# Optimization experiments

Hardware: AMD Instinct MI355X
Metric: run time of the kernel (lower is better)

Reference implementation:

```python
import jax, jax.numpy as jnp
import numpy as np
from jax import lax

DN = ('NCHW', 'OIHW', 'NCHW')


def setup_inputs() -> dict:
    key = jax.random.key(0)
    ks = jax.random.split(key, 5)
    B, C, H, W = 32, 512, 56, 56
    R = 16
    return {
        'x': jax.random.normal(ks[0], (B, C, H, W), jnp.float32),
        'w1': jax.random.normal(ks[1], (1, 3, 3, 3), jnp.float32) * 0.2,   # shared conv over (y1,y2,y4) triplet
        'w2': jax.random.normal(ks[2], (1, 1, 3, 3), jnp.float32) * 0.2,   # shared depthwise conv
        'fc1_w': jax.random.normal(ks[3], (C // R, C), jnp.float32) * 0.05,
        'fc2_w': jax.random.normal(ks[4], (C, C // R), jnp.float32) * 0.05,
    }


def reference(x, w1, w2, fc1_w, fc2_w):
    b, c, h, w = x.shape
    # multi-scale adaptive average pooling (H,W divisible by 4) + nearest upsample to 4x4
    y1 = jnp.broadcast_to(x.mean(axis=(2, 3), keepdims=True), (b, c, 4, 4))      # pool1 -> interp x4
    y2 = x.reshape(b, c, 2, h // 2, 2, w // 2).mean(axis=(3, 5))                 # [b,c,2,2]
    y2 = jnp.repeat(jnp.repeat(y2, 2, axis=2), 2, axis=3)                        # nearest interp x2 -> 4x4
    y4 = x.reshape(b, c, 4, h // 4, 4, w // 4).mean(axis=(3, 5))                 # [b,c,4,4]
    # ShareGroupConv(3c->c): out channel j sees channels (j, c+j, 2c+j) = (y1_j, y2_j, y4_j)
    t = jnp.stack([y1, y2, y4], axis=2).reshape(b * c, 3, 4, 4)
    z = lax.conv_general_dilated(t, w1, (1, 1), 'VALID', dimension_numbers=DN)   # [b*c,1,2,2]
    # ShareGroupConv(c->c, k=3, pad=1, stride=3): shared per-channel conv, 2x2 -> 1x1
    z = lax.conv_general_dilated(z, w2, (3, 3), [(1, 1), (1, 1)], dimension_numbers=DN)
    s = z.reshape(b, c)
    s = jax.nn.relu(s @ fc1_w.T) @ fc2_w.T
    s = jax.nn.sigmoid(s).reshape(b, c, 1, 1)
    return x * s
```

## Files before the change

### kernel.cpp

```cpp
#include <hip/hip_runtime.h>
#include <math.h>

#define Bn 32
#define Cn 512
#define Hn 56
#define Wn 56
#define HW (Hn*Wn)
#define NPLANE (Bn*Cn)

__global__ __launch_bounds__(256) void pool_conv_kernel(
    const float* __restrict__ x,
    const float* __restrict__ w1,
    const float* __restrict__ w2,
    float* __restrict__ s0)
{
    __shared__ float plane[HW];
    __shared__ float rs[Hn * 4];
    __shared__ float y4[16];

    const int bc = blockIdx.x;
    const int t  = threadIdx.x;
    const float* src = x + (size_t)bc * HW;

    for (int f = t; f < HW / 4; f += 256)
        ((float4*)plane)[f] = ((const float4*)src)[f];
    __syncthreads();

    if (t < Hn * 4) {
        const int h = t >> 2, j = t & 3;
        const float* row = plane + h * Wn + j * 14;
        float s = 0.f;
        #pragma unroll
        for (int e = 0; e < 14; ++e) s += row[e];
        rs[h * 4 + j] = s;
    }
    __syncthreads();

    if (t < 16) {
        const int i = t >> 2, j = t & 3;
        float s = 0.f;
        #pragma unroll
        for (int r = 0; r < 14; ++r) s += rs[(i * 14 + r) * 4 + j];
        y4[i * 4 + j] = s * (1.0f / 196.0f);
    }
    __syncthreads();

    if (t == 0) {
        float y2[2][2];
        #pragma unroll
        for (int p = 0; p < 2; ++p)
            #pragma unroll
            for (int q = 0; q < 2; ++q)
                y2[p][q] = 0.25f * (y4[(2*p)*4 + 2*q]   + y4[(2*p)*4 + 2*q+1]
                                  + y4[(2*p+1)*4 + 2*q] + y4[(2*p+1)*4 + 2*q+1]);
        const float y1 = 0.25f * (y2[0][0] + y2[0][1] + y2[1][0] + y2[1][1]);

        float z[2][2];
        #pragma unroll
        for (int oy = 0; oy < 2; ++oy)
            #pragma unroll
            for (int ox = 0; ox < 2; ++ox) {
                float acc = 0.f;
                #pragma unroll
                for (int ky = 0; ky < 3; ++ky)
                    #pragma unroll
                    for (int kx = 0; kx < 3; ++kx) {
                        const int yy = oy + ky, xx = ox + kx;
                        acc += y1                  * w1[0*9 + ky*3 + kx];
                        acc += y2[yy >> 1][xx >> 1] * w1[1*9 + ky*3 + kx];
                        acc += y4[yy*4 + xx]        * w1[2*9 + ky*3 + kx];
                    }
                z[oy][ox] = acc;
            }

        const float out = z[0][0] * w2[1*3+1] + z[0][1] * w2[1*3+2]
                        + z[1][0] * w2[2*3+1] + z[1][1] * w2[2*3+2];
        s0[bc] = out;
    }
}

__global__ __launch_bounds__(256) void fc_kernel(
    const float* __restrict__ s0,
    const float* __restrict__ fc1,
    const float* __restrict__ fc2,
    float* __restrict__ s)
{
    __shared__ float sv[Cn];
    __shared__ float hv[32];
    const int b = blockIdx.x;
    const int t = threadIdx.x;

    for (int c = t; c < Cn; c += 256) sv[c] = s0[b * Cn + c];
    __syncthreads();

    {
        const int r = t >> 3, lane8 = t & 7;
        float acc = 0.f;
        for (int c = lane8; c < Cn; c += 8) acc += sv[c] * fc1[r * Cn + c];
        acc += __shfl_xor(acc, 1);
        acc += __shfl_xor(acc, 2);
        acc += __shfl_xor(acc, 4);
        if (lane8 == 0) hv[r] = fmaxf(acc, 0.f);
    }
    __syncthreads();

    for (int c = t; c < Cn; c += 256) {
        float acc = 0.f;
        #pragma unroll
        for (int r = 0; r < 32; ++r) acc += hv[r] * fc2[c * 32 + r];
        s[b * Cn + c] = 1.0f / (1.0f + expf(-acc));
    }
}

__global__ __launch_bounds__(256) void scale_kernel(
    const float* __restrict__ x,
    const float* __restrict__ s,
    float* __restrict__ out)
{
    const int n4 = NPLANE * HW / 4;
    const int stride = gridDim.x * blockDim.x;
    for (int i = blockIdx.x * blockDim.x + threadIdx.x; i < n4; i += stride) {
        float4 v = ((const float4*)x)[i];
        const float sc = s[i / (HW / 4)];
        v.x *= sc; v.y *= sc; v.z *= sc; v.w *= sc;
        ((float4*)out)[i] = v;
    }
}

extern "C" void kernel_launch(void* const* d_in, const int* in_sizes, int n_in,
                              void* d_out, int out_size, void* d_ws, size_t ws_size,
                              hipStream_t stream) {
    const float* x   = (const float*)d_in[0];
    const float* w1  = (const float*)d_in[1];
    const float* w2  = (const float*)d_in[2];
    const float* fc1 = (const float*)d_in[3];
    const float* fc2 = (const float*)d_in[4];
    float* out = (float*)d_out;

    float* s0 = (float*)d_ws;
    float* s  = s0 + NPLANE;

    pool_conv_kernel<<<NPLANE, 256, 0, stream>>>(x, w1, w2, s0);
    fc_kernel<<<Bn, 256, 0, stream>>>(s0, fc1, fc2, s);
    scale_kernel<<<2048, 256, 0, stream>>>(x, s, out);
}
```

Baseline: 126.4 us.

## Fuse FC excitation into the scale kernel with per-block channel groups

Merges the squeeze FC layers and the broadcast scale into one kernel. Each of 2048 blocks recomputes the FC1 hidden vector for its batch, computes sigmoid scales for its 8 channels, then scales those 8 planes using nontemporal stores. This removes one launch, the intermediate scale buffer and the per-element index division. In exchange, FC1 is computed redundantly 64 times per batch.

```diff
diff --git a/kernel.cpp b/kernel.cpp
--- a/kernel.cpp
+++ b/kernel.cpp
@@ -7,6 +7,9 @@
 #define Wn 56
 #define HW (Hn*Wn)
 #define NPLANE (Bn*Cn)
+#define F4_PER_PLANE (HW/4)
+
+typedef float f4 __attribute__((ext_vector_type(4)));
 
 __global__ __launch_bounds__(256) void pool_conv_kernel(
     const float* __restrict__ x,
@@ -22,8 +25,8 @@
     const int t  = threadIdx.x;
     const float* src = x + (size_t)bc * HW;
 
-    for (int f = t; f < HW / 4; f += 256)
-        ((float4*)plane)[f] = ((const float4*)src)[f];
+    for (int f = t; f < F4_PER_PLANE; f += 256)
+        ((f4*)plane)[f] = ((const f4*)src)[f];
     __syncthreads();
 
     if (t < Hn * 4) {
@@ -66,29 +69,32 @@
                     #pragma unroll
                     for (int kx = 0; kx < 3; ++kx) {
                         const int yy = oy + ky, xx = ox + kx;
-                        acc += y1                  * w1[0*9 + ky*3 + kx];
+                        acc += y1                   * w1[0*9 + ky*3 + kx];
                         acc += y2[yy >> 1][xx >> 1] * w1[1*9 + ky*3 + kx];
                         acc += y4[yy*4 + xx]        * w1[2*9 + ky*3 + kx];
                     }
                 z[oy][ox] = acc;
             }
 
-        const float out = z[0][0] * w2[1*3+1] + z[0][1] * w2[1*3+2]
-                        + z[1][0] * w2[2*3+1] + z[1][1] * w2[2*3+2];
-        s0[bc] = out;
+        s0[bc] = z[0][0] * w2[1*3+1] + z[0][1] * w2[1*3+2]
+               + z[1][0] * w2[2*3+1] + z[1][1] * w2[2*3+2];
     }
 }
 
-__global__ __launch_bounds__(256) void fc_kernel(
+__global__ __launch_bounds__(256) void fc_scale_kernel(
+    const float* __restrict__ x,
     const float* __restrict__ s0,
     const float* __restrict__ fc1,
     const float* __restrict__ fc2,
-    float* __restrict__ s)
+    float* __restrict__ out)
 {
     __shared__ float sv[Cn];
     __shared__ float hv[32];
-    const int b = blockIdx.x;
-    const int t = threadIdx.x;
+    __shared__ float scl[8];
+
+    const int b  = blockIdx.x >> 6;
+    const int kk = blockIdx.x & 63;
+    const int t  = threadIdx.x;
 
     for (int c = t; c < Cn; c += 256) sv[c] = s0[b * Cn + c];
     __syncthreads();
@@ -104,26 +110,26 @@
     }
     __syncthreads();
 
-    for (int c = t; c < Cn; c += 256) {
+    if (t < 8) {
+        const int c = kk * 8 + t;
         float acc = 0.f;
         #pragma unroll
         for (int r = 0; r < 32; ++r) acc += hv[r] * fc2[c * 32 + r];
-        s[b * Cn + c] = 1.0f / (1.0f + expf(-acc));
+        scl[t] = 1.0f / (1.0f + expf(-acc));
     }
-}
+    __syncthreads();
 
-__global__ __launch_bounds__(256) void scale_kernel(
-    const float* __restrict__ x,
-    const float* __restrict__ s,
-    float* __restrict__ out)
-{
-    const int n4 = NPLANE * HW / 4;
-    const int stride = gridDim.x * blockDim.x;
-    for (int i = blockIdx.x * blockDim.x + threadIdx.x; i < n4; i += stride) {
-        float4 v = ((const float4*)x)[i];
-        const float sc = s[i / (HW / 4)];
-        v.x *= sc; v.y *= sc; v.z *= sc; v.w *= sc;
-        ((float4*)out)[i] = v;
+    #pragma unroll
+    for (int p = 0; p < 8; ++p) {
+        const int plane = b * Cn + kk * 8 + p;
+        const float sc = scl[p];
+        const f4* px = (const f4*)x + (size_t)plane * F4_PER_PLANE;
+        f4* po = (f4*)out + (size_t)plane * F4_PER_PLANE;
+        for (int f = t; f < F4_PER_PLANE; f += 256) {
+            f4 v = px[f];
+            v *= sc;
+            __builtin_nontemporal_store(v, po + f);
+        }
     }
 }
 
@@ -138,9 +144,7 @@
     float* out = (float*)d_out;
 
     float* s0 = (float*)d_ws;
-    float* s  = s0 + NPLANE;
 
     pool_conv_kernel<<<NPLANE, 256, 0, stream>>>(x, w1, w2, s0);
-    fc_kernel<<<Bn, 256, 0, stream>>>(s0, fc1, fc2, s);
-    scale_kernel<<<2048, 256, 0, stream>>>(x, s, out);
+    fc_scale_kernel<<<Bn * 64, 256, 0, stream>>>(x, s0, fc1, fc2, out);
 }
```

Result: faster. 108.1 us (-14.5%).
